# Kernel tuning notes

Measured on AMD Instinct MI355X. Metric: run time of the kernel, lower is better.

## Reference

```python
import math
import jax, jax.numpy as jnp
import numpy as np

B, S, D, H, FF, E, V, RH = 8, 256, 512, 8, 2048, 8, 32000, 256
MAX_PATH, MAX_VISITS = 4, 2
NEG = -1e9
DH = D // H


def _make_pe():
    # PositionalEncoding buffer (sin/cos), sliced to seq len S
    pos = np.arange(S, dtype=np.float32)[:, None]
    div = np.exp(np.arange(0, D, 2, dtype=np.float32) * (-math.log(10000.0) / D))
    pe = np.zeros((S, D), dtype=np.float32)
    pe[:, 0::2] = np.sin(pos * div)
    pe[:, 1::2] = np.cos(pos * div)
    return jnp.asarray(pe[None])  # [1,S,D]


def setup_inputs() -> dict:
    key = jax.random.key(0)
    ks = jax.random.split(key, 12)
    s = 0.02
    return dict(
        input_ids=jax.random.randint(ks[0], (B, S), 0, V),
        emb=jax.random.normal(ks[1], (V, D), jnp.float32) * s,
        pe=_make_pe(),
        Wqkv=jax.random.normal(ks[2], (E, 3 * D, D), jnp.float32) * s,
        bqkv=jnp.zeros((E, 3 * D), jnp.float32),
        Wo=jax.random.normal(ks[3], (E, D, D), jnp.float32) * s,
        bo=jnp.zeros((E, D), jnp.float32),
        W1=jax.random.normal(ks[4], (E, FF, D), jnp.float32) * s,
        b1=jnp.zeros((E, FF), jnp.float32),
        W2=jax.random.normal(ks[5], (E, D, FF), jnp.float32) * s,
        b2=jnp.zeros((E, D), jnp.float32),
        ln1_g=jnp.ones((E, D), jnp.float32), ln1_b=jnp.zeros((E, D), jnp.float32),
        ln2_g=jnp.ones((E, D), jnp.float32), ln2_b=jnp.zeros((E, D), jnp.float32),
        tag=jax.random.normal(ks[6], (E, D), jnp.float32) * 0.01,
        r_w1=jax.random.normal(ks[7], (RH, D), jnp.float32) * s,
        r_b1=jnp.zeros((RH,), jnp.float32),
        r_w2=jax.random.normal(ks[8], (E + 1, RH), jnp.float32) * s,
        r_b2=jnp.zeros((E + 1,), jnp.float32),
        lm_w=jax.random.normal(ks[9], (V, D), jnp.float32) * s,
        lm_b=jnp.zeros((V,), jnp.float32),
    )


def _ln(x, g, b):
    # per-sample gathered LayerNorm params g,b: [B,D]; x: [B,S,D]
    mu = x.mean(-1, keepdims=True)
    var = ((x - mu) ** 2).mean(-1, keepdims=True)
    return (x - mu) * jax.lax.rsqrt(var + 1e-5) * g[:, None, :] + b[:, None, :]


def _expert(x, idx, Wqkv, bqkv, Wo, bo, W1, b1, W2, b2, g1, be1, g2, be2, tag):
    # post-norm TransformerEncoderLayer (eval mode, dropout off) with per-sample expert params
    qkv = jnp.einsum('bsd,bfd->bsf', x, Wqkv[idx]) + bqkv[idx][:, None, :]
    q, k, v = jnp.split(qkv, 3, axis=-1)
    q = q.reshape(B, S, H, DH)
    k = k.reshape(B, S, H, DH)
    v = v.reshape(B, S, H, DH)
    att = jax.nn.softmax(jnp.einsum('bqhd,bkhd->bhqk', q, k) / math.sqrt(DH), axis=-1)
    ctx = jnp.einsum('bhqk,bkhd->bqhd', att, v).reshape(B, S, D)
    attn_out = jnp.einsum('bsd,bod->bso', ctx, Wo[idx]) + bo[idx][:, None, :]
    x = _ln(x + attn_out, g1[idx], be1[idx])
    hid = jax.nn.relu(jnp.einsum('bsd,bfd->bsf', x, W1[idx]) + b1[idx][:, None, :])
    ff = jnp.einsum('bsf,bdf->bsd', hid, W2[idx]) + b2[idx][:, None, :]
    x = _ln(x + ff, g2[idx], be2[idx])
    return x + tag[idx][:, None, :]  # + specialization_tag


def reference(input_ids, emb, pe, Wqkv, bqkv, Wo, bo, W1, b1, W2, b2,
              ln1_g, ln1_b, ln2_g, ln2_b, tag, r_w1, r_b1, r_w2, r_b2, lm_w, lm_b):
    pad_mask = (jnp.arange(V) != 0).astype(emb.dtype)[:, None]  # padding_idx=0 row is zero
    rep = (emb * pad_mask)[input_ids] * math.sqrt(D) + pe[:, :S]
    visits = jnp.zeros((B, E), jnp.int32)
    active = jnp.ones((B,), bool)
    ent_total = jnp.asarray(0.0, rep.dtype)
    for _ in range(MAX_PATH):
        summary = rep.mean(1)  # [B,D]
        h = jax.nn.relu(summary @ r_w1.T + r_b1)
        logits = h @ r_w2.T + r_b2  # [B,E+1], last slot = terminate
        logits = jnp.concatenate(
            [jnp.where(visits >= MAX_VISITS, NEG, logits[:, :E]), logits[:, E:]], axis=1)
        probs = jax.nn.softmax(logits, axis=-1)
        ent = -jnp.sum(probs * jnp.log(probs + 1e-9), axis=-1)
        cnt = jnp.sum(active)
        ent_total = ent_total + jnp.where(
            cnt > 0, jnp.sum(ent * active) / jnp.maximum(cnt, 1).astype(ent.dtype), 0.0)
        choice = jnp.argmax(logits, axis=-1)       # eval mode: hard argmax
        go = active & (choice < E)                 # samples routed to an expert this step
        idx = jnp.where(go, choice, 0)
        visits = visits + jax.nn.one_hot(idx, E, dtype=jnp.int32) * go[:, None].astype(jnp.int32)
        new_rep = _expert(rep, idx, Wqkv, bqkv, Wo, bo, W1, b1, W2, b2,
                          ln1_g, ln1_b, ln2_g, ln2_b, tag)
        rep = jnp.where(go[:, None, None], new_rep, rep)  # terminated/inactive reps frozen
        active = go
    logits_lm = rep @ lm_w.T + lm_b  # [B,S,V]
    return logits_lm, ent_total
```

## Files before the change

kernel.cpp:

```cpp
#include <hip/hip_runtime.h>
#include <hip/hip_bf16.h>

#define NB 8
#define NS 256
#define ND 512
#define NH 8
#define NDH 64
#define NFF 2048
#define NE 8
#define NV 32000
#define NRH 256
#define MAXV 2
#define NEGV (-1e9f)

typedef __attribute__((ext_vector_type(8))) short short8;
typedef __attribute__((ext_vector_type(4))) float f32x4;

__device__ __forceinline__ unsigned short f2bf(float x) {
  unsigned int u = __float_as_uint(x);
  u = (u + 0x7fffu + ((u >> 16) & 1u)) >> 16;
  return (unsigned short)u;
}

__device__ __forceinline__ void gload16(const unsigned short* g, unsigned short* l) {
  __builtin_amdgcn_global_load_lds(
      (const __attribute__((address_space(1))) unsigned int*)g,
      (__attribute__((address_space(3))) unsigned int*)l, 16, 0, 0);
}

__device__ __forceinline__ int swzc(int lane) {
  return (lane & 3) ^ ((lane >> 3) & 3);
}

__device__ __forceinline__ void cast8(const float* s, unsigned short* d, int j) {
  const float4* s4 = (const float4*)s;
  float4 a = s4[j * 2], b = s4[j * 2 + 1];
  short8 v;
  v[0] = (short)f2bf(a.x); v[1] = (short)f2bf(a.y);
  v[2] = (short)f2bf(a.z); v[3] = (short)f2bf(a.w);
  v[4] = (short)f2bf(b.x); v[5] = (short)f2bf(b.y);
  v[6] = (short)f2bf(b.z); v[7] = (short)f2bf(b.w);
  *(short8*)&d[(size_t)j * 8] = v;
}

__global__ __launch_bounds__(256) void k_cast5e(
    const float* s0, unsigned short* d0, int n0,
    const float* s1, unsigned short* d1, int n1,
    const float* s2, unsigned short* d2, int n2,
    const float* s3, unsigned short* d3, int n3,
    const float* s4, unsigned short* d4, int n4,
    int nbcast,
    const int* __restrict__ ids, const float* __restrict__ emb,
    const float* __restrict__ pe, float* __restrict__ rep,
    unsigned short* __restrict__ repb, float* __restrict__ partial,
    int* visits, int* active, float* entp) {
  if (blockIdx.x == 0) {
    if (threadIdx.x < NB * NE) visits[threadIdx.x] = 0;
    if (threadIdx.x < NB) active[threadIdx.x] = 1;
    if (threadIdx.x == 0) *entp = 0.f;
  }
  if ((int)blockIdx.x >= nbcast) {
    int j2 = blockIdx.x - nbcast;
    int rg = j2 & 15, b = j2 >> 4;
    int t = threadIdx.x;
    int c0 = t, c1 = t + 256;
    float p0 = 0.f, p1 = 0.f;
    for (int row = 0; row < 16; ++row) {
      int s = rg * 16 + row;
      int id = ids[b * NS + s];
      float sc = (id != 0) ? 22.627416997969522f : 0.f;
      float v0 = emb[(size_t)id * ND + c0] * sc + pe[(size_t)s * ND + c0];
      float v1 = emb[(size_t)id * ND + c1] * sc + pe[(size_t)s * ND + c1];
      size_t base = ((size_t)b * NS + s) * ND;
      rep[base + c0] = v0; rep[base + c1] = v1;
      repb[base + c0] = f2bf(v0); repb[base + c1] = f2bf(v1);
      p0 += v0; p1 += v1;
    }
    float* pp = partial + ((size_t)b * 16 + rg) * ND;
    pp[c0] = p0; pp[c1] = p1;
    return;
  }
  int j = blockIdx.x * 256 + threadIdx.x;
  if (j < n0) { cast8(s0, d0, j); return; }
  j -= n0;
  if (j < n1) { cast8(s1, d1, j); return; }
  j -= n1;
  if (j < n2) { cast8(s2, d2, j); return; }
  j -= n2;
  if (j < n3) { cast8(s3, d3, j); return; }
  j -= n3;
  if (j < n4) cast8(s4, d4, j);
}

__global__ __launch_bounds__(256) void k_router(const float* __restrict__ partial,
                                                const float* __restrict__ rw1,
                                                const float* __restrict__ rb1,
                                                const float* __restrict__ rw2,
                                                const float* __restrict__ rb2,
                                                int* visits, int* active,
                                                int* idx, int* go, float* ent_total) {
  __shared__ float sm[NB][ND];
  __shared__ float h[NB][NRH];
  __shared__ float lg[NB][NE + 1];
  int t = threadIdx.x;
  for (int i = t; i < NB * ND; i += 256) {
    int bb = i >> 9, d = i & 511;
    const float* pp = partial + ((size_t)bb * 16) * ND + d;
    float s = 0.f;
#pragma unroll
    for (int rg = 0; rg < 16; ++rg) s += pp[(size_t)rg * ND];
    sm[bb][d] = s * (1.f / NS);
  }
  __syncthreads();
  {
    const float* w = rw1 + (size_t)t * ND;
    float acc[NB];
#pragma unroll
    for (int b = 0; b < NB; ++b) acc[b] = rb1[t];
    for (int d = 0; d < ND; ++d) {
      float wv = w[d];
#pragma unroll
      for (int b = 0; b < NB; ++b) acc[b] += sm[b][d] * wv;
    }
#pragma unroll
    for (int b = 0; b < NB; ++b) h[b][t] = fmaxf(acc[b], 0.f);
  }
  __syncthreads();
  if (t < NB * (NE + 1)) {
    int b = t / (NE + 1), e = t % (NE + 1);
    const float* w = rw2 + e * NRH;
    float a = rb2[e];
    for (int r = 0; r < NRH; ++r) a += h[b][r] * w[r];
    lg[b][e] = a;
  }
  __syncthreads();
  if (t == 0) {
    int aprev[NB];
    int cnt = 0;
    for (int b = 0; b < NB; ++b) { aprev[b] = active[b]; cnt += aprev[b]; }
    float entsum = 0.f;
    for (int b = 0; b < NB; ++b) {
      float l[NE + 1];
      for (int e = 0; e < NE; ++e)
        l[e] = (visits[b * NE + e] >= MAXV) ? NEGV : lg[b][e];
      l[NE] = lg[b][NE];
      float m = l[0];
      for (int e = 1; e <= NE; ++e) m = fmaxf(m, l[e]);
      float z = 0.f, p[NE + 1];
      for (int e = 0; e <= NE; ++e) { p[e] = __expf(l[e] - m); z += p[e]; }
      float zi = 1.f / z, ent = 0.f;
      for (int e = 0; e <= NE; ++e) {
        float pp = p[e] * zi;
        ent -= pp * __logf(pp + 1e-9f);
      }
      if (aprev[b]) entsum += ent;
      int ch = 0; float bm = l[0];
      for (int e = 1; e <= NE; ++e) if (l[e] > bm) { bm = l[e]; ch = e; }
      int g = (aprev[b] && ch < NE) ? 1 : 0;
      int ix = g ? ch : 0;
      visits[b * NE + ix] += g;
      idx[b] = ix; go[b] = g; active[b] = g;
    }
    if (cnt > 0) *ent_total += entsum / (float)cnt;
  }
}

template <int OUT, int RELU>
__global__ __launch_bounds__(256) void k_gemmN128(
    const unsigned short* __restrict__ Aall, int sa,
    const unsigned short* __restrict__ Wall, const float* __restrict__ ball,
    unsigned short* __restrict__ Uall, int so, int N, int K,
    unsigned short* __restrict__ Qb, unsigned short* __restrict__ Kb,
    unsigned short* __restrict__ Vt,
    const int* __restrict__ go, const int* __restrict__ idx) {
  int b = blockIdx.z;
  if (!go[b]) return;
  int t = threadIdx.x;
  int lane = t & 63, w = t >> 6;
  int wm = (w >> 1) * 32, wn = (w & 1) * 64;
  int bm = blockIdx.x * 64, bn = blockIdx.y * 128;
  int lrow = (lane >> 4) * 4, lcol = lane & 15;
  const unsigned short* A = Aall + (size_t)b * sa;
  const unsigned short* W = Wall + (size_t)idx[b] * N * K;
  const float* bias = ball + (size_t)idx[b] * N;

  __shared__ __align__(16) unsigned short As[2][64][32];
  __shared__ __align__(16) unsigned short Bs[2][128][32];
  f32x4 acc[2][4];
#pragma unroll
  for (int i = 0; i < 2; ++i)
#pragma unroll
    for (int j = 0; j < 4; ++j) acc[i][j] = (f32x4){0.f, 0.f, 0.f, 0.f};

  const unsigned short* ga = A + (size_t)(bm + w * 16 + (lane >> 2)) * K + swzc(lane) * 8;
  const unsigned short* gb = W + (size_t)(bn + w * 32 + (lane >> 2)) * K + swzc(lane) * 8;

  gload16(ga, &As[0][w * 16][0]);
  gload16(gb, &Bs[0][w * 32][0]);
  gload16(gb + 16 * (size_t)K, &Bs[0][w * 32 + 16][0]);
  __syncthreads();

  int nk = K >> 5;
  int row0 = lane & 15;
  int cs = ((lane >> 4) ^ ((row0 >> 1) & 3)) * 8;
  for (int it = 0; it < nk; ++it) {
    int cur = it & 1;
    if (it + 1 < nk) {
      gload16(ga + (it + 1) * 32, &As[cur ^ 1][w * 16][0]);
      gload16(gb + (it + 1) * 32, &Bs[cur ^ 1][w * 32][0]);
      gload16(gb + (it + 1) * 32 + 16 * (size_t)K, &Bs[cur ^ 1][w * 32 + 16][0]);
    }
    short8 a[2], bfr[4];
#pragma unroll
    for (int mf = 0; mf < 2; ++mf)
      a[mf] = *(const short8*)&As[cur][wm + mf * 16 + row0][cs];
#pragma unroll
    for (int nf = 0; nf < 4; ++nf)
      bfr[nf] = *(const short8*)&Bs[cur][wn + nf * 16 + row0][cs];
#pragma unroll
    for (int mf = 0; mf < 2; ++mf)
#pragma unroll
      for (int nf = 0; nf < 4; ++nf)
        acc[mf][nf] = __builtin_amdgcn_mfma_f32_16x16x32_bf16(a[mf], bfr[nf], acc[mf][nf], 0, 0, 0);
    __syncthreads();
  }

  if (OUT == 2) {
    int seg = bn >> 9;
#pragma unroll
    for (int nf = 0; nf < 4; ++nf) {
      int col = bn + wn + nf * 16 + lcol;
      float bv = bias[col];
      if (seg < 2) {
        unsigned short* dst = (seg == 0) ? Qb : Kb;
        int cc = col - seg * 512;
#pragma unroll
        for (int mf = 0; mf < 2; ++mf)
#pragma unroll
          for (int r = 0; r < 4; ++r) {
            int row = bm + wm + mf * 16 + lrow + r;
            dst[((size_t)b * NS + row) * ND + cc] = f2bf(acc[mf][nf][r] + bv);
          }
      } else {
        int dcol = col - 1024;
#pragma unroll
        for (int mf = 0; mf < 2; ++mf) {
          int s0 = bm + wm + mf * 16 + lrow;
          unsigned long long pk =
              (unsigned long long)f2bf(acc[mf][nf][0] + bv) |
              ((unsigned long long)f2bf(acc[mf][nf][1] + bv) << 16) |
              ((unsigned long long)f2bf(acc[mf][nf][2] + bv) << 32) |
              ((unsigned long long)f2bf(acc[mf][nf][3] + bv) << 48);
          *(unsigned long long*)&Vt[((size_t)b * 512 + dcol) * 256 + s0] = pk;
        }
      }
    }
  } else {
#pragma unroll
    for (int nf = 0; nf < 4; ++nf) {
      int col = bn + wn + nf * 16 + lcol;
      float bv = bias[col];
#pragma unroll
      for (int mf = 0; mf < 2; ++mf) {
#pragma unroll
        for (int r = 0; r < 4; ++r) {
          int row = bm + wm + mf * 16 + lrow + r;
          float v = acc[mf][nf][r] + bv;
          if (RELU) v = fmaxf(v, 0.f);
          Uall[(size_t)b * so + (size_t)row * N + col] = f2bf(v);
        }
      }
    }
  }
}

template <int NCH>
__global__ __launch_bounds__(256) void k_gemm64sk(
    const unsigned short* __restrict__ Aall, int sa,
    const unsigned short* __restrict__ Wall,
    float* __restrict__ Pall, int N, int K,
    const int* __restrict__ go, const int* __restrict__ idx) {
  int b = blockIdx.z;
  if (!go[b]) return;
  int t = threadIdx.x;
  int lane = t & 63, w = t >> 6;
  int wm = (w >> 1) * 32, wn = (w & 1) * 32;
  int kc = blockIdx.x >> 2;
  int bm = (blockIdx.x & 3) * 64, bn = blockIdx.y * 64;
  int KC = K / NCH;
  int lrow = (lane >> 4) * 4, lcol = lane & 15;
  const unsigned short* A = Aall + (size_t)b * sa + kc * KC;
  const unsigned short* W = Wall + (size_t)idx[b] * N * K + kc * KC;

  __shared__ __align__(16) unsigned short As[2][64][32];
  __shared__ __align__(16) unsigned short Bs[2][64][32];
  f32x4 acc[2][2];
#pragma unroll
  for (int i = 0; i < 2; ++i)
#pragma unroll
    for (int j = 0; j < 2; ++j) acc[i][j] = (f32x4){0.f, 0.f, 0.f, 0.f};

  const unsigned short* ga = A + (size_t)(bm + w * 16 + (lane >> 2)) * K + swzc(lane) * 8;
  const unsigned short* gb = W + (size_t)(bn + w * 16 + (lane >> 2)) * K + swzc(lane) * 8;

  gload16(ga, &As[0][w * 16][0]);
  gload16(gb, &Bs[0][w * 16][0]);
  __syncthreads();

  int nk = KC >> 5;
  int row0 = lane & 15;
  int cs = ((lane >> 4) ^ ((row0 >> 1) & 3)) * 8;
  for (int it = 0; it < nk; ++it) {
    int cur = it & 1;
    if (it + 1 < nk) {
      gload16(ga + (it + 1) * 32, &As[cur ^ 1][w * 16][0]);
      gload16(gb + (it + 1) * 32, &Bs[cur ^ 1][w * 16][0]);
    }
    short8 a[2], bfr[2];
#pragma unroll
    for (int mf = 0; mf < 2; ++mf)
      a[mf] = *(const short8*)&As[cur][wm + mf * 16 + row0][cs];
#pragma unroll
    for (int nf = 0; nf < 2; ++nf)
      bfr[nf] = *(const short8*)&Bs[cur][wn + nf * 16 + row0][cs];
#pragma unroll
    for (int mf = 0; mf < 2; ++mf)
#pragma unroll
      for (int nf = 0; nf < 2; ++nf)
        acc[mf][nf] = __builtin_amdgcn_mfma_f32_16x16x32_bf16(a[mf], bfr[nf], acc[mf][nf], 0, 0, 0);
    __syncthreads();
  }

  float* P = Pall + ((size_t)kc * NB + b) * ((size_t)NS * N);
#pragma unroll
  for (int nf = 0; nf < 2; ++nf) {
    int col = bn + wn + nf * 16 + lcol;
#pragma unroll
    for (int mf = 0; mf < 2; ++mf)
#pragma unroll
      for (int r = 0; r < 4; ++r)
        P[(size_t)(bm + wm + mf * 16 + lrow + r) * N + col] = acc[mf][nf][r];
  }
}

__global__ __launch_bounds__(256) void k_attn2(const unsigned short* __restrict__ Qb,
                                               const unsigned short* __restrict__ Kb,
                                               const unsigned short* __restrict__ Vt,
                                               unsigned short* __restrict__ ctxb,
                                               const int* __restrict__ go) {
  int b = blockIdx.z, h = blockIdx.y, qt = blockIdx.x;
  if (!go[b]) return;
  int t = threadIdx.x;
  __shared__ __align__(16) unsigned short lds0[16384];
  __shared__ __align__(16) unsigned short lds1[16384];
  int lane = t & 63, w = t >> 6, g = lane >> 4, c = lane & 15;

#pragma unroll
  for (int i = 0; i < 8; ++i) {
    int task = i * 256 + t;
    int k = task >> 3, cc = task & 7;
    short8 v = *(const short8*)&Kb[((size_t)b * NS + k) * ND + h * NDH + cc * 8];
    *(short8*)&lds0[k * 64 + ((cc * 8) ^ ((k & 7) << 3))] = v;
  }
#pragma unroll
  for (int i = 0; i < 8; ++i) {
    int task = i * 256 + t;
    int d = task >> 5, kc = task & 31;
    short8 v = *(const short8*)&Vt[((size_t)b * 512 + h * NDH + d) * 256 + kc * 8];
    *(short8*)&lds1[d * 256 + ((kc * 8) ^ ((d & 7) << 3))] = v;
  }
  short8 qf[2];
  {
    const unsigned short* qp = Qb + ((size_t)b * NS + qt * 64 + w * 16 + c) * ND + h * NDH;
    qf[0] = *(const short8*)&qp[g * 8];
    qf[1] = *(const short8*)&qp[32 + g * 8];
  }
  __syncthreads();

  f32x4 sacc[16];
#pragma unroll
  for (int mf = 0; mf < 16; ++mf) sacc[mf] = (f32x4){0.f, 0.f, 0.f, 0.f};
#pragma unroll
  for (int mf = 0; mf < 16; ++mf) {
#pragma unroll
    for (int kd = 0; kd < 2; ++kd) {
      int row = mf * 16 + c;
      short8 kf = *(const short8*)&lds0[row * 64 + ((kd * 32 + g * 8) ^ ((row & 7) << 3))];
      sacc[mf] = __builtin_amdgcn_mfma_f32_16x16x32_bf16(kf, qf[kd], sacc[mf], 0, 0, 0);
    }
  }
  __syncthreads();

  float mx = -3.4e38f;
#pragma unroll
  for (int mf = 0; mf < 16; ++mf) {
#pragma unroll
    for (int r = 0; r < 4; ++r) {
      sacc[mf][r] *= 0.125f;
      mx = fmaxf(mx, sacc[mf][r]);
    }
  }
  mx = fmaxf(mx, __shfl_xor(mx, 16));
  mx = fmaxf(mx, __shfl_xor(mx, 32));
  float sum = 0.f;
#pragma unroll
  for (int mf = 0; mf < 16; ++mf)
#pragma unroll
    for (int r = 0; r < 4; ++r) {
      float p = __expf(sacc[mf][r] - mx);
      sacc[mf][r] = p;
      sum += p;
    }
  sum += __shfl_xor(sum, 16);
  sum += __shfl_xor(sum, 32);
  float zi = 1.f / sum;

  int q_l = w * 16 + c;
#pragma unroll
  for (int mf = 0; mf < 16; ++mf) {
    unsigned long long pk =
        (unsigned long long)f2bf(sacc[mf][0] * zi) |
        ((unsigned long long)f2bf(sacc[mf][1] * zi) << 16) |
        ((unsigned long long)f2bf(sacc[mf][2] * zi) << 32) |
        ((unsigned long long)f2bf(sacc[mf][3] * zi) << 48);
    *(unsigned long long*)&lds0[q_l * 256 + ((mf * 16 + g * 4) ^ ((q_l & 7) << 3))] = pk;
  }

  f32x4 cacc[4];
#pragma unroll
  for (int nf = 0; nf < 4; ++nf) cacc[nf] = (f32x4){0.f, 0.f, 0.f, 0.f};
#pragma unroll
  for (int ks = 0; ks < 8; ++ks) {
    int prow = w * 16 + c;
    short8 pf = *(const short8*)&lds0[prow * 256 + ((ks * 32 + g * 8) ^ ((prow & 7) << 3))];
#pragma unroll
    for (int nf = 0; nf < 4; ++nf) {
      int vrow = nf * 16 + c;
      short8 vf = *(const short8*)&lds1[vrow * 256 + ((ks * 32 + g * 8) ^ ((vrow & 7) << 3))];
      cacc[nf] = __builtin_amdgcn_mfma_f32_16x16x32_bf16(pf, vf, cacc[nf], 0, 0, 0);
    }
  }
#pragma unroll
  for (int nf = 0; nf < 4; ++nf)
#pragma unroll
    for (int r = 0; r < 4; ++r)
      ctxb[((size_t)b * NS + qt * 64 + w * 16 + g * 4 + r) * ND + h * NDH + nf * 16 + c] =
          f2bf(cacc[nf][r]);
}

template <int NCH, int TAG, int SUMP>
__global__ __launch_bounds__(256) void k_ln_red(
    const float* __restrict__ res, const float* __restrict__ part,
    const float* __restrict__ gbias,
    const float* __restrict__ gall, const float* __restrict__ beall,
    const float* __restrict__ tagall,
    float* __restrict__ outf, unsigned short* __restrict__ outb,
    float* __restrict__ sump,
    const int* __restrict__ go, const int* __restrict__ idx) {
  int b = blockIdx.y;
  if (!go[b]) return;
  int rg = blockIdx.x;
  int w = threadIdx.x >> 6, l = threadIdx.x & 63;
  int ix = idx[b];
  int d = l * 8;
  float gb8[8], gg[8], bb[8];
  {
    float4 a0 = *(const float4*)&gbias[ix * ND + d];
    float4 a1 = *(const float4*)&gbias[ix * ND + d + 4];
    gb8[0] = a0.x; gb8[1] = a0.y; gb8[2] = a0.z; gb8[3] = a0.w;
    gb8[4] = a1.x; gb8[5] = a1.y; gb8[6] = a1.z; gb8[7] = a1.w;
    float4 g0 = *(const float4*)&gall[ix * ND + d];
    float4 g1 = *(const float4*)&gall[ix * ND + d + 4];
    gg[0] = g0.x; gg[1] = g0.y; gg[2] = g0.z; gg[3] = g0.w;
    gg[4] = g1.x; gg[5] = g1.y; gg[6] = g1.z; gg[7] = g1.w;
    float4 b0 = *(const float4*)&beall[ix * ND + d];
    float4 b1 = *(const float4*)&beall[ix * ND + d + 4];
    bb[0] = b0.x; bb[1] = b0.y; bb[2] = b0.z; bb[3] = b0.w;
    bb[4] = b1.x; bb[5] = b1.y; bb[6] = b1.z; bb[7] = b1.w;
    if (TAG) {
      float4 t0 = *(const float4*)&tagall[ix * ND + d];
      float4 t1 = *(const float4*)&tagall[ix * ND + d + 4];
      bb[0] += t0.x; bb[1] += t0.y; bb[2] += t0.z; bb[3] += t0.w;
      bb[4] += t1.x; bb[5] += t1.y; bb[6] += t1.z; bb[7] += t1.w;
    }
  }
  float ps[8] = {0.f, 0.f, 0.f, 0.f, 0.f, 0.f, 0.f, 0.f};
  const size_t CSTRIDE = (size_t)NB * NS * ND;
  for (int rr = 0; rr < 4; ++rr) {
    int s = rg * 16 + w * 4 + rr;
    size_t base = ((size_t)b * NS + s) * ND;
    float4 x0 = *(const float4*)&res[base + d];
    float4 x1 = *(const float4*)&res[base + d + 4];
    float v[8] = {x0.x + gb8[0], x0.y + gb8[1], x0.z + gb8[2], x0.w + gb8[3],
                  x1.x + gb8[4], x1.y + gb8[5], x1.z + gb8[6], x1.w + gb8[7]};
#pragma unroll
    for (int c = 0; c < NCH; ++c) {
      const float* pc = part + c * CSTRIDE + base;
      float4 p0 = *(const float4*)&pc[d];
      float4 p1 = *(const float4*)&pc[d + 4];
      v[0] += p0.x; v[1] += p0.y; v[2] += p0.z; v[3] += p0.w;
      v[4] += p1.x; v[5] += p1.y; v[6] += p1.z; v[7] += p1.w;
    }
    float sum = 0.f;
#pragma unroll
    for (int j = 0; j < 8; ++j) sum += v[j];
#pragma unroll
    for (int off = 1; off < 64; off <<= 1) sum += __shfl_xor(sum, off);
    float mu = sum * (1.f / ND);
    float var = 0.f;
#pragma unroll
    for (int j = 0; j < 8; ++j) { v[j] -= mu; var += v[j] * v[j]; }
#pragma unroll
    for (int off = 1; off < 64; off <<= 1) var += __shfl_xor(var, off);
    float rs = rsqrtf(var * (1.f / ND) + 1e-5f);
    float o[8];
    short8 ob;
#pragma unroll
    for (int j = 0; j < 8; ++j) {
      o[j] = v[j] * rs * gg[j] + bb[j];
      if (SUMP) ps[j] += o[j];
      ob[j] = (short)f2bf(o[j]);
    }
    *(float4*)&outf[base + d] = (float4){o[0], o[1], o[2], o[3]};
    *(float4*)&outf[base + d + 4] = (float4){o[4], o[5], o[6], o[7]};
    *(short8*)&outb[base + d] = ob;
  }
  if (SUMP) {
    __shared__ float pl[4][ND];
#pragma unroll
    for (int j = 0; j < 8; ++j) pl[w][d + j] = ps[j];
    __syncthreads();
    if (w == 0) {
      float* pp = sump + ((size_t)b * 16 + rg) * ND;
#pragma unroll
      for (int j = 0; j < 8; ++j)
        pp[d + j] = pl[0][d + j] + pl[1][d + j] + pl[2][d + j] + pl[3][d + j];
    }
  }
}

__global__ __launch_bounds__(512, 2) void k_lmhead256(const unsigned short* __restrict__ Ab,
                                                      const unsigned short* __restrict__ Wb,
                                                      const float* __restrict__ bias,
                                                      float* __restrict__ out,
                                                      const float* __restrict__ entp) {
  if (blockIdx.x == 0 && threadIdx.x == 0)
    out[(size_t)NB * NS * NV] = *entp;
  int id = blockIdx.x;
  int swz = (id & 7) * 125 + (id >> 3);
  int bm = (swz % 8) * 256;
  int bn = (swz / 8) * 256;

  __shared__ __align__(16) unsigned short As[2][256][32];
  __shared__ __align__(16) unsigned short Bs[2][256][32];
  int t = threadIdx.x;
  int lane = t & 63, w = t >> 6;
  int wm = (w >> 2) * 128, wn = (w & 3) * 64;
  f32x4 acc[8][4];
#pragma unroll
  for (int i = 0; i < 8; ++i)
#pragma unroll
    for (int j = 0; j < 4; ++j) acc[i][j] = (f32x4){0.f, 0.f, 0.f, 0.f};

  const unsigned short* ga = Ab + (size_t)(bm + w * 32 + (lane >> 2)) * ND + swzc(lane) * 8;
  const unsigned short* gb = Wb + (size_t)(bn + w * 32 + (lane >> 2)) * ND + swzc(lane) * 8;

  gload16(ga, &As[0][w * 32][0]);
  gload16(ga + 16 * ND, &As[0][w * 32 + 16][0]);
  gload16(gb, &Bs[0][w * 32][0]);
  gload16(gb + 16 * ND, &Bs[0][w * 32 + 16][0]);
  __syncthreads();

  int row0 = lane & 15;
  int cs = ((lane >> 4) ^ ((row0 >> 1) & 3)) * 8;
  for (int it = 0; it < 16; ++it) {
    int cur = it & 1;
    if (it < 15) {
      int k0 = (it + 1) * 32;
      gload16(ga + k0, &As[cur ^ 1][w * 32][0]);
      gload16(ga + k0 + 16 * ND, &As[cur ^ 1][w * 32 + 16][0]);
      gload16(gb + k0, &Bs[cur ^ 1][w * 32][0]);
      gload16(gb + k0 + 16 * ND, &Bs[cur ^ 1][w * 32 + 16][0]);
    }
    short8 a[8], bfr[4];
#pragma unroll
    for (int mf = 0; mf < 8; ++mf)
      a[mf] = *(const short8*)&As[cur][wm + mf * 16 + row0][cs];
#pragma unroll
    for (int nf = 0; nf < 4; ++nf)
      bfr[nf] = *(const short8*)&Bs[cur][wn + nf * 16 + row0][cs];
#pragma unroll
    for (int mf = 0; mf < 8; ++mf)
#pragma unroll
      for (int nf = 0; nf < 4; ++nf)
        acc[mf][nf] = __builtin_amdgcn_mfma_f32_16x16x32_bf16(a[mf], bfr[nf], acc[mf][nf], 0, 0, 0);
    __syncthreads();
  }
  int lrow = (lane >> 4) * 4, lcol = lane & 15;
#pragma unroll
  for (int nf = 0; nf < 4; ++nf) {
    int col = bn + wn + nf * 16 + lcol;
    float bv = bias[col];
#pragma unroll
    for (int mf = 0; mf < 8; ++mf) {
#pragma unroll
      for (int r = 0; r < 4; ++r) {
        int row = bm + wm + mf * 16 + lrow + r;
        out[(size_t)row * NV + col] = acc[mf][nf][r] + bv;
      }
    }
  }
}

extern "C" void kernel_launch(void* const* d_in, const int* in_sizes, int n_in,
                              void* d_out, int out_size, void* d_ws, size_t ws_size,
                              hipStream_t stream) {
  const int* ids   = (const int*)d_in[0];
  const float* emb = (const float*)d_in[1];
  const float* pe  = (const float*)d_in[2];
  const float* Wqkv = (const float*)d_in[3];
  const float* bqkv = (const float*)d_in[4];
  const float* Wo   = (const float*)d_in[5];
  const float* bo   = (const float*)d_in[6];
  const float* W1   = (const float*)d_in[7];
  const float* b1   = (const float*)d_in[8];
  const float* W2   = (const float*)d_in[9];
  const float* b2   = (const float*)d_in[10];
  const float* g1   = (const float*)d_in[11];
  const float* be1  = (const float*)d_in[12];
  const float* g2   = (const float*)d_in[13];
  const float* be2  = (const float*)d_in[14];
  const float* tag  = (const float*)d_in[15];
  const float* rw1  = (const float*)d_in[16];
  const float* rb1  = (const float*)d_in[17];
  const float* rw2  = (const float*)d_in[18];
  const float* rb2  = (const float*)d_in[19];
  const float* lmw  = (const float*)d_in[20];
  const float* lmb  = (const float*)d_in[21];
  float* out = (float*)d_out;

  float* ws = (float*)d_ws;
  size_t o = 0;
  float* rep = ws + o;  o += (size_t)NB * NS * ND;
  float* x1  = ws + o;  o += (size_t)NB * NS * ND;
  float* partk = ws + o; o += (size_t)4 * NB * NS * ND;
  float* partial = ws + o; o += (size_t)NB * 16 * ND;
  int* visits = (int*)(ws + o); o += 1024;
  int* active = visits + NB * NE;
  int* idx = active + NB;
  int* go = idx + NB;
  float* entp = (float*)(go + NB);

  unsigned short* us = (unsigned short*)(ws + o);
  size_t uo = 0;
  unsigned short* rep_b = us + uo; uo += (size_t)NB * NS * ND;
  unsigned short* x1_b  = us + uo; uo += (size_t)NB * NS * ND;
  unsigned short* ctx_b = us + uo; uo += (size_t)NB * NS * ND;
  unsigned short* Qb    = us + uo; uo += (size_t)NB * NS * ND;
  unsigned short* Kb    = us + uo; uo += (size_t)NB * NS * ND;
  unsigned short* Vt    = us + uo; uo += (size_t)NB * NS * ND;
  unsigned short* hid_b = us + uo; uo += (size_t)NB * NS * NFF;
  unsigned short* Wqkv_b = us + uo; uo += (size_t)NE * 3 * ND * ND;
  unsigned short* Wo_b   = us + uo; uo += (size_t)NE * ND * ND;
  unsigned short* W1_b   = us + uo; uo += (size_t)NE * NFF * ND;
  unsigned short* W2_b   = us + uo; uo += (size_t)NE * ND * NFF;
  unsigned short* lmw_b  = us + uo; uo += (size_t)NV * ND;

  {
    int n0 = NE * 3 * ND * ND / 8, n1 = NE * ND * ND / 8, n2 = NE * NFF * ND / 8,
        n3 = NE * ND * NFF / 8, n4 = NV * ND / 8;
    int nbcast = (n0 + n1 + n2 + n3 + n4) / 256;
    k_cast5e<<<nbcast + 16 * NB, 256, 0, stream>>>(
        Wqkv, Wqkv_b, n0, Wo, Wo_b, n1, W1, W1_b, n2, W2, W2_b, n3, lmw, lmw_b, n4,
        nbcast, ids, emb, pe, rep, rep_b, partial, visits, active, entp);
  }

  for (int step = 0; step < 4; ++step) {
    k_router<<<1, 256, 0, stream>>>(partial, rw1, rb1, rw2, rb2,
                                    visits, active, idx, go, entp);
    k_gemmN128<2, 0><<<dim3(4, 12, NB), 256, 0, stream>>>(
        rep_b, NS * ND, Wqkv_b, bqkv, nullptr, 0, 3 * ND, ND,
        Qb, Kb, Vt, go, idx);
    k_attn2<<<dim3(4, NH, NB), 256, 0, stream>>>(Qb, Kb, Vt, ctx_b, go);
    k_gemm64sk<2><<<dim3(8, 8, NB), 256, 0, stream>>>(
        ctx_b, NS * ND, Wo_b, partk, ND, ND, go, idx);
    k_ln_red<2, 0, 0><<<dim3(16, NB), 256, 0, stream>>>(
        rep, partk, bo, g1, be1, nullptr, x1, x1_b, nullptr, go, idx);
    k_gemmN128<1, 1><<<dim3(4, 16, NB), 256, 0, stream>>>(
        x1_b, NS * ND, W1_b, b1, hid_b, NS * NFF, NFF, ND,
        nullptr, nullptr, nullptr, go, idx);
    k_gemm64sk<4><<<dim3(16, 8, NB), 256, 0, stream>>>(
        hid_b, NS * NFF, W2_b, partk, ND, NFF, go, idx);
    k_ln_red<4, 1, 1><<<dim3(16, NB), 256, 0, stream>>>(
        x1, partk, b2, g2, be2, tag, rep, rep_b, partial, go, idx);
  }

  k_lmhead256<<<1000, 512, 0, stream>>>(rep_b, lmw_b, lmb, out, entp);
}
```

Baseline: 602.9 us.

## Unify expert GEMMs into 64x64 triple-buffered kernel with explicit vmcnt waits

```diff
diff --git a/kernel.cpp b/kernel.cpp
--- a/kernel.cpp
+++ b/kernel.cpp
@@ -165,11 +165,12 @@
   }
 }
 
-template <int OUT, int RELU>
-__global__ __launch_bounds__(256) void k_gemmN128(
+template <int OUT, int RELU, int SK>
+__global__ __launch_bounds__(256) void k_gemm64p(
     const unsigned short* __restrict__ Aall, int sa,
     const unsigned short* __restrict__ Wall, const float* __restrict__ ball,
-    unsigned short* __restrict__ Uall, int so, int N, int K,
+    float* __restrict__ Pall, unsigned short* __restrict__ Uall, int so,
+    int N, int K,
     unsigned short* __restrict__ Qb, unsigned short* __restrict__ Kb,
     unsigned short* __restrict__ Vt,
     const int* __restrict__ go, const int* __restrict__ idx) {
@@ -177,58 +178,65 @@
   if (!go[b]) return;
   int t = threadIdx.x;
   int lane = t & 63, w = t >> 6;
-  int wm = (w >> 1) * 32, wn = (w & 1) * 64;
-  int bm = blockIdx.x * 64, bn = blockIdx.y * 128;
+  int wm = (w >> 1) * 32, wn = (w & 1) * 32;
+  int kc = blockIdx.x >> 2;
+  int bm = (blockIdx.x & 3) * 64, bn = blockIdx.y * 64;
+  int KC = K / SK;
   int lrow = (lane >> 4) * 4, lcol = lane & 15;
-  const unsigned short* A = Aall + (size_t)b * sa;
-  const unsigned short* W = Wall + (size_t)idx[b] * N * K;
-  const float* bias = ball + (size_t)idx[b] * N;
-
-  __shared__ __align__(16) unsigned short As[2][64][32];
-  __shared__ __align__(16) unsigned short Bs[2][128][32];
-  f32x4 acc[2][4];
+  const unsigned short* A = Aall + (size_t)b * sa + kc * KC;
+  const unsigned short* W = Wall + (size_t)idx[b] * N * K + kc * KC;
+
+  __shared__ __align__(16) unsigned short As[3][64][32];
+  __shared__ __align__(16) unsigned short Bs[3][64][32];
+  f32x4 acc[2][2];
 #pragma unroll
   for (int i = 0; i < 2; ++i)
 #pragma unroll
-    for (int j = 0; j < 4; ++j) acc[i][j] = (f32x4){0.f, 0.f, 0.f, 0.f};
+    for (int j = 0; j < 2; ++j) acc[i][j] = (f32x4){0.f, 0.f, 0.f, 0.f};
 
   const unsigned short* ga = A + (size_t)(bm + w * 16 + (lane >> 2)) * K + swzc(lane) * 8;
-  const unsigned short* gb = W + (size_t)(bn + w * 32 + (lane >> 2)) * K + swzc(lane) * 8;
-
-  gload16(ga, &As[0][w * 16][0]);
-  gload16(gb, &Bs[0][w * 32][0]);
-  gload16(gb + 16 * (size_t)K, &Bs[0][w * 32 + 16][0]);
-  __syncthreads();
-
-  int nk = K >> 5;
+  const unsigned short* gb = W + (size_t)(bn + w * 16 + (lane >> 2)) * K + swzc(lane) * 8;
+
+#define ISSUE64(slot, kt)                        \
+  gload16(ga + (kt) * 32, &As[slot][w * 16][0]); \
+  gload16(gb + (kt) * 32, &Bs[slot][w * 16][0]);
+
+  int nk = KC >> 5;
+  ISSUE64(0, 0)
+  ISSUE64(1, 1)
+  ISSUE64(2, 2)
+
   int row0 = lane & 15;
   int cs = ((lane >> 4) ^ ((row0 >> 1) & 3)) * 8;
   for (int it = 0; it < nk; ++it) {
-    int cur = it & 1;
-    if (it + 1 < nk) {
-      gload16(ga + (it + 1) * 32, &As[cur ^ 1][w * 16][0]);
-      gload16(gb + (it + 1) * 32, &Bs[cur ^ 1][w * 32][0]);
-      gload16(gb + (it + 1) * 32 + 16 * (size_t)K, &Bs[cur ^ 1][w * 32 + 16][0]);
-    }
-    short8 a[2], bfr[4];
+    int rem = nk - 1 - it;
+    if (rem >= 2)      asm volatile("s_waitcnt vmcnt(4)" ::: "memory");
+    else if (rem == 1) asm volatile("s_waitcnt vmcnt(2)" ::: "memory");
+    else               asm volatile("s_waitcnt vmcnt(0)" ::: "memory");
+    asm volatile("s_barrier" ::: "memory");
+    int sl = it % 3;
+    short8 a[2], bfr[2];
 #pragma unroll
     for (int mf = 0; mf < 2; ++mf)
-      a[mf] = *(const short8*)&As[cur][wm + mf * 16 + row0][cs];
-#pragma unroll
-    for (int nf = 0; nf < 4; ++nf)
-      bfr[nf] = *(const short8*)&Bs[cur][wn + nf * 16 + row0][cs];
+      a[mf] = *(const short8*)&As[sl][wm + mf * 16 + row0][cs];
+#pragma unroll
+    for (int nf = 0; nf < 2; ++nf)
+      bfr[nf] = *(const short8*)&Bs[sl][wn + nf * 16 + row0][cs];
 #pragma unroll
     for (int mf = 0; mf < 2; ++mf)
 #pragma unroll
-      for (int nf = 0; nf < 4; ++nf)
+      for (int nf = 0; nf < 2; ++nf)
         acc[mf][nf] = __builtin_amdgcn_mfma_f32_16x16x32_bf16(a[mf], bfr[nf], acc[mf][nf], 0, 0, 0);
-    __syncthreads();
-  }
+    asm volatile("s_barrier" ::: "memory");
+    if (it + 3 < nk) { ISSUE64(sl, it + 3) }
+  }
+#undef ISSUE64
 
   if (OUT == 2) {
+    const float* bias = ball + (size_t)idx[b] * N;
     int seg = bn >> 9;
 #pragma unroll
-    for (int nf = 0; nf < 4; ++nf) {
+    for (int nf = 0; nf < 2; ++nf) {
       int col = bn + wn + nf * 16 + lcol;
       float bv = bias[col];
       if (seg < 2) {
@@ -255,9 +263,10 @@
         }
       }
     }
-  } else {
-#pragma unroll
-    for (int nf = 0; nf < 4; ++nf) {
+  } else if (OUT == 1) {
+    const float* bias = ball + (size_t)idx[b] * N;
+#pragma unroll
+    for (int nf = 0; nf < 2; ++nf) {
       int col = bn + wn + nf * 16 + lcol;
       float bv = bias[col];
 #pragma unroll
@@ -271,75 +280,17 @@
         }
       }
     }
-  }
-}
-
-template <int NCH>
-__global__ __launch_bounds__(256) void k_gemm64sk(
-    const unsigned short* __restrict__ Aall, int sa,
-    const unsigned short* __restrict__ Wall,
-    float* __restrict__ Pall, int N, int K,
-    const int* __restrict__ go, const int* __restrict__ idx) {
-  int b = blockIdx.z;
-  if (!go[b]) return;
-  int t = threadIdx.x;
-  int lane = t & 63, w = t >> 6;
-  int wm = (w >> 1) * 32, wn = (w & 1) * 32;
-  int kc = blockIdx.x >> 2;
-  int bm = (blockIdx.x & 3) * 64, bn = blockIdx.y * 64;
-  int KC = K / NCH;
-  int lrow = (lane >> 4) * 4, lcol = lane & 15;
-  const unsigned short* A = Aall + (size_t)b * sa + kc * KC;
-  const unsigned short* W = Wall + (size_t)idx[b] * N * K + kc * KC;
-
-  __shared__ __align__(16) unsigned short As[2][64][32];
-  __shared__ __align__(16) unsigned short Bs[2][64][32];
-  f32x4 acc[2][2];
-#pragma unroll
-  for (int i = 0; i < 2; ++i)
-#pragma unroll
-    for (int j = 0; j < 2; ++j) acc[i][j] = (f32x4){0.f, 0.f, 0.f, 0.f};
-
-  const unsigned short* ga = A + (size_t)(bm + w * 16 + (lane >> 2)) * K + swzc(lane) * 8;
-  const unsigned short* gb = W + (size_t)(bn + w * 16 + (lane >> 2)) * K + swzc(lane) * 8;
-
-  gload16(ga, &As[0][w * 16][0]);
-  gload16(gb, &Bs[0][w * 16][0]);
-  __syncthreads();
-
-  int nk = KC >> 5;
-  int row0 = lane & 15;
-  int cs = ((lane >> 4) ^ ((row0 >> 1) & 3)) * 8;
-  for (int it = 0; it < nk; ++it) {
-    int cur = it & 1;
-    if (it + 1 < nk) {
-      gload16(ga + (it + 1) * 32, &As[cur ^ 1][w * 16][0]);
-      gload16(gb + (it + 1) * 32, &Bs[cur ^ 1][w * 16][0]);
-    }
-    short8 a[2], bfr[2];
-#pragma unroll
-    for (int mf = 0; mf < 2; ++mf)
-      a[mf] = *(const short8*)&As[cur][wm + mf * 16 + row0][cs];
-#pragma unroll
-    for (int nf = 0; nf < 2; ++nf)
-      bfr[nf] = *(const short8*)&Bs[cur][wn + nf * 16 + row0][cs];
-#pragma unroll
-    for (int mf = 0; mf < 2; ++mf)
-#pragma unroll
-      for (int nf = 0; nf < 2; ++nf)
-        acc[mf][nf] = __builtin_amdgcn_mfma_f32_16x16x32_bf16(a[mf], bfr[nf], acc[mf][nf], 0, 0, 0);
-    __syncthreads();
-  }
-
-  float* P = Pall + ((size_t)kc * NB + b) * ((size_t)NS * N);
-#pragma unroll
-  for (int nf = 0; nf < 2; ++nf) {
-    int col = bn + wn + nf * 16 + lcol;
-#pragma unroll
-    for (int mf = 0; mf < 2; ++mf)
-#pragma unroll
-      for (int r = 0; r < 4; ++r)
-        P[(size_t)(bm + wm + mf * 16 + lrow + r) * N + col] = acc[mf][nf][r];
+  } else {
+    float* P = Pall + ((size_t)kc * NB + b) * ((size_t)NS * N);
+#pragma unroll
+    for (int nf = 0; nf < 2; ++nf) {
+      int col = bn + wn + nf * 16 + lcol;
+#pragma unroll
+      for (int mf = 0; mf < 2; ++mf)
+#pragma unroll
+        for (int r = 0; r < 4; ++r)
+          P[(size_t)(bm + wm + mf * 16 + lrow + r) * N + col] = acc[mf][nf][r];
+    }
   }
 }
 
@@ -565,37 +516,39 @@
   const unsigned short* ga = Ab + (size_t)(bm + w * 32 + (lane >> 2)) * ND + swzc(lane) * 8;
   const unsigned short* gb = Wb + (size_t)(bn + w * 32 + (lane >> 2)) * ND + swzc(lane) * 8;
 
-  gload16(ga, &As[0][w * 32][0]);
-  gload16(ga + 16 * ND, &As[0][w * 32 + 16][0]);
-  gload16(gb, &Bs[0][w * 32][0]);
-  gload16(gb + 16 * ND, &Bs[0][w * 32 + 16][0]);
-  __syncthreads();
+#define ISSUEL(slot, kt)                                           \
+  gload16(ga + (kt) * 32, &As[slot][w * 32][0]);                   \
+  gload16(ga + (kt) * 32 + 16 * ND, &As[slot][w * 32 + 16][0]);    \
+  gload16(gb + (kt) * 32, &Bs[slot][w * 32][0]);                   \
+  gload16(gb + (kt) * 32 + 16 * ND, &Bs[slot][w * 32 + 16][0]);
+
+  ISSUEL(0, 0)
+  ISSUEL(1, 1)
 
   int row0 = lane & 15;
   int cs = ((lane >> 4) ^ ((row0 >> 1) & 3)) * 8;
   for (int it = 0; it < 16; ++it) {
-    int cur = it & 1;
-    if (it < 15) {
-      int k0 = (it + 1) * 32;
-      gload16(ga + k0, &As[cur ^ 1][w * 32][0]);
-      gload16(ga + k0 + 16 * ND, &As[cur ^ 1][w * 32 + 16][0]);
-      gload16(gb + k0, &Bs[cur ^ 1][w * 32][0]);
-      gload16(gb + k0 + 16 * ND, &Bs[cur ^ 1][w * 32 + 16][0]);
-    }
+    if (it < 15) asm volatile("s_waitcnt vmcnt(4)" ::: "memory");
+    else         asm volatile("s_waitcnt vmcnt(0)" ::: "memory");
+    asm volatile("s_barrier" ::: "memory");
+    int sl = it & 1;
     short8 a[8], bfr[4];
 #pragma unroll
     for (int mf = 0; mf < 8; ++mf)
-      a[mf] = *(const short8*)&As[cur][wm + mf * 16 + row0][cs];
+      a[mf] = *(const short8*)&As[sl][wm + mf * 16 + row0][cs];
 #pragma unroll
     for (int nf = 0; nf < 4; ++nf)
-      bfr[nf] = *(const short8*)&Bs[cur][wn + nf * 16 + row0][cs];
+      bfr[nf] = *(const short8*)&Bs[sl][wn + nf * 16 + row0][cs];
 #pragma unroll
     for (int mf = 0; mf < 8; ++mf)
 #pragma unroll
       for (int nf = 0; nf < 4; ++nf)
         acc[mf][nf] = __builtin_amdgcn_mfma_f32_16x16x32_bf16(a[mf], bfr[nf], acc[mf][nf], 0, 0, 0);
-    __syncthreads();
-  }
+    asm volatile("s_barrier" ::: "memory");
+    if (it + 2 < 16) { ISSUEL(sl, it + 2) }
+  }
+#undef ISSUEL
+
   int lrow = (lane >> 4) * 4, lcol = lane & 15;
 #pragma unroll
   for (int nf = 0; nf < 4; ++nf) {
@@ -678,19 +631,21 @@
   for (int step = 0; step < 4; ++step) {
     k_router<<<1, 256, 0, stream>>>(partial, rw1, rb1, rw2, rb2,
                                     visits, active, idx, go, entp);
-    k_gemmN128<2, 0><<<dim3(4, 12, NB), 256, 0, stream>>>(
-        rep_b, NS * ND, Wqkv_b, bqkv, nullptr, 0, 3 * ND, ND,
+    k_gemm64p<2, 0, 1><<<dim3(4, 24, NB), 256, 0, stream>>>(
+        rep_b, NS * ND, Wqkv_b, bqkv, nullptr, nullptr, 0, 3 * ND, ND,
         Qb, Kb, Vt, go, idx);
     k_attn2<<<dim3(4, NH, NB), 256, 0, stream>>>(Qb, Kb, Vt, ctx_b, go);
-    k_gemm64sk<2><<<dim3(8, 8, NB), 256, 0, stream>>>(
-        ctx_b, NS * ND, Wo_b, partk, ND, ND, go, idx);
+    k_gemm64p<0, 0, 2><<<dim3(8, 8, NB), 256, 0, stream>>>(
+        ctx_b, NS * ND, Wo_b, nullptr, partk, nullptr, 0, ND, ND,
+        nullptr, nullptr, nullptr, go, idx);
     k_ln_red<2, 0, 0><<<dim3(16, NB), 256, 0, stream>>>(
         rep, partk, bo, g1, be1, nullptr, x1, x1_b, nullptr, go, idx);
-    k_gemmN128<1, 1><<<dim3(4, 16, NB), 256, 0, stream>>>(
-        x1_b, NS * ND, W1_b, b1, hid_b, NS * NFF, NFF, ND,
+    k_gemm64p<1, 1, 1><<<dim3(4, 32, NB), 256, 0, stream>>>(
+        x1_b, NS * ND, W1_b, b1, nullptr, hid_b, NS * NFF, NFF, ND,
         nullptr, nullptr, nullptr, go, idx);
-    k_gemm64sk<4><<<dim3(16, 8, NB), 256, 0, stream>>>(
-        hid_b, NS * NFF, W2_b, partk, ND, NFF, go, idx);
+    k_gemm64p<0, 0, 4><<<dim3(16, 8, NB), 256, 0, stream>>>(
+        hid_b, NS * NFF, W2_b, nullptr, partk, nullptr, 0, ND, NFF,
+        nullptr, nullptr, nullptr, go, idx);
     k_ln_red<4, 1, 1><<<dim3(16, NB), 256, 0, stream>>>(
         x1, partk, b2, g2, be2, tag, rep, rep_b, partial, go, idx);
   }
```

Result: faster. 587.8 us (-2.5%).
